# Kernel optimization log

Measured on AMD Instinct MI355X. Metric: run time of the kernel, lower is better.

## Reference

```python
import jax, jax.numpy as jnp
import numpy as np

DIM = 96
NUM_EXPERTS = 4
TOP_K = 1

def setup_inputs() -> dict:
    key = jax.random.key(0)
    ks = jax.random.split(key, 8)
    B, C, H, W = 16, DIM, 128, 128
    E = NUM_EXPERTS
    x = jax.random.normal(ks[0], (B, C, H, W), dtype=jnp.float32)
    # per-expert depthwise 3x3 conv (groups=C): torch weight [C,1,3,3]
    dw_w = jax.random.normal(ks[1], (E, C, 1, 3, 3), dtype=jnp.float32) * 0.1
    dw_b = jax.random.normal(ks[2], (E, C), dtype=jnp.float32) * 0.05
    # per-expert pointwise 1x1 conv: torch weight [C,C,1,1]
    pw_w = jax.random.normal(ks[3], (E, C, C, 1, 1), dtype=jnp.float32) * 0.1
    pw_b = jax.random.normal(ks[4], (E, C), dtype=jnp.float32) * 0.05
    # router linear: torch weight [E, C]
    router_w = jax.random.normal(ks[5], (E, C), dtype=jnp.float32) * 0.1
    router_b = jax.random.normal(ks[6], (E,), dtype=jnp.float32) * 0.05
    return {"x": x, "dw_w": dw_w, "dw_b": dw_b, "pw_w": pw_w, "pw_b": pw_b,
            "router_w": router_w, "router_b": router_b}

def _conv(x, w, groups):
    return jax.lax.conv_general_dilated(
        x, w, window_strides=(1, 1), padding='SAME',
        dimension_numbers=('NCHW', 'OIHW', 'NCHW'),
        feature_group_count=groups)

def _expert(x, dw_w, dw_b, pw_w, pw_b):
    C = x.shape[1]
    h = _conv(x, dw_w, groups=C) + dw_b[None, :, None, None]   # depthwise 3x3
    h = jax.nn.gelu(h, approximate=False)                       # torch GELU (erf)
    return _conv(h, pw_w, groups=1) + pw_b[None, :, None, None] # 1x1 conv

def reference(x, dw_w, dw_b, pw_w, pw_b, router_w, router_b):
    B, C, H, W = x.shape
    E = dw_w.shape[0]
    # router: global avg pool -> linear -> softmax
    pooled = jnp.mean(x, axis=(2, 3))                            # [B, C]
    logits = pooled @ router_w.T + router_b                      # [B, E]
    router_weights = jax.nn.softmax(logits, axis=-1)
    top_weights, top_indices = jax.lax.top_k(router_weights, TOP_K)  # [B, k]
    top_weights = top_weights / (jnp.sum(top_weights, axis=-1, keepdims=True) + 1e-8)
    # run all experts (faithful to the original, which does not dispatch)
    expert_outputs = jnp.stack(
        [_expert(x, dw_w[e], dw_b[e], pw_w[e], pw_b[e]) for e in range(E)],
        axis=1)                                                  # [B, E, C, H, W]
    # scatter top-k weights into dense gates [B, E]
    gates = jnp.zeros((B, E), dtype=x.dtype)
    gates = gates.at[jnp.arange(B)[:, None], top_indices].set(top_weights)
    return jnp.einsum('bechw,be->bchw', expert_outputs, gates)
```

## Files before the change

kernel.cpp:

```cpp
#include <hip/hip_runtime.h>
#include <math.h>

#define DIM 96
#define NE 4
#define HH 128
#define WW 128
#define BB 16
#define KP 24
#define HSROW (KP * 2)
#define HSBUF (WW * HSROW)
#define PWROW 192

typedef __attribute__((ext_vector_type(8))) __bf16 bf16x8;
typedef __attribute__((ext_vector_type(4))) float floatx4;

__device__ __forceinline__ unsigned short f2bf(float f) {
    unsigned u = __builtin_bit_cast(unsigned, f);
    unsigned r = u + 0x7FFFu + ((u >> 16) & 1u);
    return (unsigned short)(r >> 16);
}
__device__ __forceinline__ unsigned pack2(float a, float b) {
    return (unsigned)f2bf(a) | ((unsigned)f2bf(b) << 16);
}

__device__ __forceinline__ float gelu_erf(float h) {
    const float x = h * 0.70710678118654752f;
    const float a = fabsf(x);
    const float t = __builtin_amdgcn_rcpf(__builtin_fmaf(0.3275911f, a, 1.0f));
    float p = __builtin_fmaf(1.061405429f, t, -1.453152027f);
    p = __builtin_fmaf(p, t, 1.421413741f);
    p = __builtin_fmaf(p, t, -0.284496736f);
    p = __builtin_fmaf(p, t, 0.254829592f);
    p *= t;
    const float e = __expf(-x * x);
    float erfv = __builtin_fmaf(-p, e, 1.0f);
    erfv = copysignf(erfv, x);
    return 0.5f * h * (1.0f + erfv);
}

__global__ __launch_bounds__(256) void pool_kernel(const float* __restrict__ x,
                                                   float* __restrict__ pooled) {
    const int bc = blockIdx.x;
    const float4* p = (const float4*)(x + (size_t)bc * (HH * WW));
    const int t = threadIdx.x;
    float s = 0.f;
#pragma unroll
    for (int k = 0; k < (HH * WW / 4) / 256; ++k) {
        float4 v = p[t + k * 256];
        s += v.x + v.y + v.z + v.w;
    }
#pragma unroll
    for (int off = 32; off; off >>= 1) s += __shfl_down(s, off, 64);
    __shared__ float ls[4];
    if ((t & 63) == 0) ls[t >> 6] = s;
    __syncthreads();
    if (t == 0) pooled[bc] = (ls[0] + ls[1] + ls[2] + ls[3]) * (1.0f / (HH * WW));
}

__global__ void router_kernel(const float* __restrict__ pooled,
                              const float* __restrict__ rw,
                              const float* __restrict__ rb,
                              float* __restrict__ gate, int* __restrict__ sel) {
    const int b = threadIdx.x;
    if (b >= BB) return;
    float logits[NE];
#pragma unroll
    for (int e = 0; e < NE; ++e) {
        float s = rb[e];
        for (int c = 0; c < DIM; ++c) s += pooled[b * DIM + c] * rw[e * DIM + c];
        logits[e] = s;
    }
    float m = logits[0];
    int mi = 0;
#pragma unroll
    for (int e = 1; e < NE; ++e)
        if (logits[e] > m) { m = logits[e]; mi = e; }
    float denom = 0.f;
#pragma unroll
    for (int e = 0; e < NE; ++e) denom += expf(logits[e] - m);
    float w = 1.0f / denom;
    gate[b] = w / (w + 1e-8f);
    sel[b] = mi;
}

__device__ __forceinline__ void issue_sub(const float* __restrict__ x, int b,
                                          int cbase, int cg, int rr0, int r,
                                          int rr2, int p4, float4 f[2][3]) {
#pragma unroll
    for (int u = 0; u < 2; ++u) {
        const float* pl = x + (size_t)(b * DIM + cbase + cg * 2 + u) * (HH * WW);
        f[u][0] = *(const float4*)(pl + rr0 * WW + p4);
        f[u][1] = *(const float4*)(pl + r   * WW + p4);
        f[u][2] = *(const float4*)(pl + rr2 * WW + p4);
    }
}

__device__ __forceinline__ void compute_sub(const float4 f[2][3],
                                            const float (*dwc)[12], int cb,
                                            int cg, float lmask, float rmask,
                                            unsigned char* hsbuf, int p4,
                                            unsigned swz) {
    float hq[2][4];
#pragma unroll
    for (int u = 0; u < 2; ++u) {
        const int c = cb + cg * 2 + u;
        const float4 wA = *(const float4*)&dwc[c][0];
        const float4 wB = *(const float4*)&dwc[c][4];
        const float4 wC = *(const float4*)&dwc[c][8];
        float h0 = wC.y, h1 = wC.y, h2 = wC.y, h3 = wC.y;
#pragma unroll
        for (int row = 0; row < 3; ++row) {
            const float ta = (row == 0) ? wA.x : ((row == 1) ? wA.w : wB.z);
            const float tb = (row == 0) ? wA.y : ((row == 1) ? wB.x : wB.w);
            const float tc = (row == 0) ? wA.z : ((row == 1) ? wB.y : wC.x);
            const float4 f4 = f[u][row];
            const float vl = __shfl_up(f4.w, 1, 32) * lmask;
            const float vr = __shfl_down(f4.x, 1, 32) * rmask;
            h0 = __builtin_fmaf(ta, vl,   __builtin_fmaf(tb, f4.x, __builtin_fmaf(tc, f4.y, h0)));
            h1 = __builtin_fmaf(ta, f4.x, __builtin_fmaf(tb, f4.y, __builtin_fmaf(tc, f4.z, h1)));
            h2 = __builtin_fmaf(ta, f4.y, __builtin_fmaf(tb, f4.z, __builtin_fmaf(tc, f4.w, h2)));
            h3 = __builtin_fmaf(ta, f4.z, __builtin_fmaf(tb, f4.w, __builtin_fmaf(tc, vr, h3)));
        }
        hq[u][0] = gelu_erf(h0);
        hq[u][1] = gelu_erf(h1);
        hq[u][2] = gelu_erf(h2);
        hq[u][3] = gelu_erf(h3);
    }
    const unsigned wb0 = (unsigned)(p4 * HSROW + cg * 4);
#pragma unroll
    for (int j = 0; j < 4; ++j) {
        const unsigned off = (wb0 + (unsigned)j * HSROW) ^ swz;
        *(unsigned*)(hsbuf + off) = pack2(hq[0][j], hq[1][j]);
    }
}

__global__ __launch_bounds__(256, 3) void moe_main(
    const float* __restrict__ x, const float* __restrict__ dw_w,
    const float* __restrict__ dw_b, const float* __restrict__ pw_w,
    const float* __restrict__ pw_b, const float* __restrict__ gate,
    const int* __restrict__ sel, float* __restrict__ out) {
    __shared__ __align__(16) unsigned char pwb[DIM * PWROW];
    __shared__ __align__(16) unsigned char hsb[4 * HSBUF];
    __shared__ float dwc[DIM][12];

    const int t = threadIdx.x;
    const unsigned bid = blockIdx.x;
    const int xcd = bid & 7;
    const int s = bid >> 3;
    const int b = s & 15;
    const int r = xcd * 16 + (s >> 4);
    const int e = sel[b];
    const float g = gate[b];

    const int lane = t & 63, w = t >> 6;
    const int wm = w & 1, wn = w >> 1;
    const int ln = lane & 15, kg = lane >> 4;
    const int cobase = wm * 48, pxbase = wn * 64;

    const int g32 = t & 31;
    const int p4 = g32 * 4;
    const int cg = t >> 5;
    const unsigned swz = (unsigned)((g32 & 7) << 4);
    const float lmask = (p4 == 0) ? 0.f : 1.f;
    const float rmask = (p4 == 124) ? 0.f : 1.f;

    const float m0 = (r > 0) ? 1.f : 0.f;
    const float m2 = (r < HH - 1) ? 1.f : 0.f;
    const int rr0 = (r > 0) ? r - 1 : 0;
    const int rr2 = (r < HH - 1) ? r + 1 : HH - 1;

    float4 fA[2][3], fB[2][3];
    issue_sub(x, b, 0, cg, rr0, r, rr2, p4, fA);
    issue_sub(x, b, 16, cg, rr0, r, rr2, p4, fB);

#pragma unroll
    for (int i = 0; i < 18; ++i) {
        const int u = i * 256 + t;
        const int co = u / 48, kp = u - co * 48;
        const float2 v = *(const float2*)(pw_w +
            ((size_t)e * DIM + co) * DIM + kp * 2);
        *(unsigned*)(pwb + ((unsigned)(co * PWROW + kp * 4) ^
                            (unsigned)((co & 7) << 4))) = pack2(v.x, v.y);
    }
    for (int j = t; j < DIM * 12; j += 256) {
        const int c = j / 12, q = j - c * 12;
        float v = 0.f;
        if (q < 9) {
            v = dw_w[((size_t)e * DIM + c) * 9 + q];
            if (q < 3) v *= m0;
            if (q >= 6) v *= m2;
        } else if (q == 9) v = dw_b[e * DIM + c];
        dwc[c][q] = v;
    }
    __syncthreads();

    floatx4 acc[3][4];
#pragma unroll
    for (int i = 0; i < 3; ++i)
#pragma unroll
        for (int j = 0; j < 4; ++j) acc[i][j] = (floatx4){0.f, 0.f, 0.f, 0.f};

#pragma unroll
    for (int pair = 0; pair < 3; ++pair) {
        const int cb = pair * 32;
        unsigned char* h0 = hsb + (unsigned)((pair & 1) * 2) * HSBUF;
        unsigned char* h1 = h0 + HSBUF;
        compute_sub(fA, dwc, cb, cg, lmask, rmask, h0, p4, swz);
        if (pair < 2) issue_sub(x, b, cb + 32, cg, rr0, r, rr2, p4, fA);
        compute_sub(fB, dwc, cb + 16, cg, lmask, rmask, h1, p4, swz);
        if (pair < 2) issue_sub(x, b, cb + 48, cg, rr0, r, rr2, p4, fB);
        __syncthreads();

        const unsigned qbase = (unsigned)((pair & 1) * 2 + (kg >> 1)) * HSBUF;
        bf16x8 af[3], bfr[4];
#pragma unroll
        for (int mf = 0; mf < 3; ++mf) {
            const int co = cobase + mf * 16 + ln;
            af[mf] = *(const bf16x8*)(pwb +
                ((unsigned)(co * PWROW + pair * 64 + kg * 16) ^
                 (unsigned)((co & 7) << 4)));
        }
#pragma unroll
        for (int nf = 0; nf < 4; ++nf) {
            const int pxv = pxbase + nf * 16 + ln;
            const unsigned boff = (unsigned)((pxv * HSROW + (kg & 1) * 16) ^
                                             (((pxv >> 2) & 7) << 4));
            bfr[nf] = *(const bf16x8*)(hsb + qbase + boff);
        }
#pragma unroll
        for (int mf = 0; mf < 3; ++mf)
#pragma unroll
            for (int nf = 0; nf < 4; ++nf)
                acc[mf][nf] = __builtin_amdgcn_mfma_f32_16x16x32_bf16(
                    af[mf], bfr[nf], acc[mf][nf], 0, 0, 0);
    }

#pragma unroll
    for (int mf = 0; mf < 3; ++mf) {
#pragma unroll
        for (int rr = 0; rr < 4; ++rr) {
            const int co = cobase + mf * 16 + kg * 4 + rr;
            const float bias = pw_b[e * DIM + co];
            float* orow = out + ((size_t)(b * DIM + co) * HH + r) * WW;
#pragma unroll
            for (int nf = 0; nf < 4; ++nf)
                orow[pxbase + nf * 16 + ln] = (acc[mf][nf][rr] + bias) * g;
        }
    }
}

extern "C" void kernel_launch(void* const* d_in, const int* in_sizes, int n_in,
                              void* d_out, int out_size, void* d_ws, size_t ws_size,
                              hipStream_t stream) {
    const float* x    = (const float*)d_in[0];
    const float* dw_w = (const float*)d_in[1];
    const float* dw_b = (const float*)d_in[2];
    const float* pw_w = (const float*)d_in[3];
    const float* pw_b = (const float*)d_in[4];
    const float* rw   = (const float*)d_in[5];
    const float* rb   = (const float*)d_in[6];
    float* out = (float*)d_out;

    float* pooled = (float*)d_ws;
    float* gate = pooled + BB * DIM;
    int* sel = (int*)(gate + BB);

    pool_kernel<<<BB * DIM, 256, 0, stream>>>(x, pooled);
    router_kernel<<<1, 64, 0, stream>>>(pooled, rw, rb, gate, sel);
    moe_main<<<HH * BB, 256, 0, stream>>>(x, dw_w, dw_b, pw_w, pw_b, gate, sel, out);
}
```

Baseline: 77.28 us.

## Process two output rows per block to reuse halo rows and pointwise weights

Each block now computes a strip of two image rows instead of one. It loads 4 input rows per channel instead of 3 per row, which cuts redundant halo reads, and it halves how often the pointwise weights are staged into LDS per output. The grid shrinks to half as many blocks and the MFMA accumulator tile doubles to 3x8. Single-buffered LDS needs an extra barrier, and the higher register pressure may lower occupancy under launch_bounds(256,3).

```diff
diff --git a/kernel.cpp b/kernel.cpp
--- a/kernel.cpp
+++ b/kernel.cpp
@@ -6,9 +6,8 @@
 #define HH 128
 #define WW 128
 #define BB 16
-#define KP 24
-#define HSROW (KP * 2)
-#define HSBUF (WW * HSROW)
+#define HSROW 48
+#define HSBUF (256 * HSROW)
 #define PWROW 192
 
 typedef __attribute__((ext_vector_type(8))) __bf16 bf16x8;
@@ -83,54 +82,92 @@
     sel[b] = mi;
 }
 
-__device__ __forceinline__ void issue_sub(const float* __restrict__ x, int b,
-                                          int cbase, int cg, int rr0, int r,
-                                          int rr2, int p4, float4 f[2][3]) {
+__device__ __forceinline__ void issue_sub2(const float* __restrict__ x, int b,
+                                           int cbase, int cg, int rm1, int r0,
+                                           int rp2, int p4, float4 f[2][4]) {
 #pragma unroll
     for (int u = 0; u < 2; ++u) {
         const float* pl = x + (size_t)(b * DIM + cbase + cg * 2 + u) * (HH * WW);
-        f[u][0] = *(const float4*)(pl + rr0 * WW + p4);
-        f[u][1] = *(const float4*)(pl + r   * WW + p4);
-        f[u][2] = *(const float4*)(pl + rr2 * WW + p4);
-    }
-}
-
-__device__ __forceinline__ void compute_sub(const float4 f[2][3],
-                                            const float (*dwc)[12], int cb,
-                                            int cg, float lmask, float rmask,
-                                            unsigned char* hsbuf, int p4,
-                                            unsigned swz) {
-    float hq[2][4];
+        f[u][0] = *(const float4*)(pl + rm1 * WW + p4);
+        f[u][1] = *(const float4*)(pl + r0 * WW + p4);
+        f[u][2] = *(const float4*)(pl + (r0 + 1) * WW + p4);
+        f[u][3] = *(const float4*)(pl + rp2 * WW + p4);
+    }
+}
+
+__device__ __forceinline__ void compute_sub2(const float4 f[2][4],
+                                             const float (*dwc)[12], int cb,
+                                             int cg, float lmask, float rmask,
+                                             float mTop, float mBot,
+                                             unsigned char* hsbuf, int p4,
+                                             unsigned swz) {
+    float hA[2][4], hB[2][4];
 #pragma unroll
     for (int u = 0; u < 2; ++u) {
         const int c = cb + cg * 2 + u;
         const float4 wA = *(const float4*)&dwc[c][0];
         const float4 wB = *(const float4*)&dwc[c][4];
         const float4 wC = *(const float4*)&dwc[c][8];
-        float h0 = wC.y, h1 = wC.y, h2 = wC.y, h3 = wC.y;
-#pragma unroll
-        for (int row = 0; row < 3; ++row) {
-            const float ta = (row == 0) ? wA.x : ((row == 1) ? wA.w : wB.z);
-            const float tb = (row == 0) ? wA.y : ((row == 1) ? wB.x : wB.w);
-            const float tc = (row == 0) ? wA.z : ((row == 1) ? wB.y : wC.x);
-            const float4 f4 = f[u][row];
-            const float vl = __shfl_up(f4.w, 1, 32) * lmask;
-            const float vr = __shfl_down(f4.x, 1, 32) * rmask;
-            h0 = __builtin_fmaf(ta, vl,   __builtin_fmaf(tb, f4.x, __builtin_fmaf(tc, f4.y, h0)));
-            h1 = __builtin_fmaf(ta, f4.x, __builtin_fmaf(tb, f4.y, __builtin_fmaf(tc, f4.z, h1)));
-            h2 = __builtin_fmaf(ta, f4.y, __builtin_fmaf(tb, f4.z, __builtin_fmaf(tc, f4.w, h2)));
-            h3 = __builtin_fmaf(ta, f4.z, __builtin_fmaf(tb, f4.w, __builtin_fmaf(tc, vr, h3)));
-        }
-        hq[u][0] = gelu_erf(h0);
-        hq[u][1] = gelu_erf(h1);
-        hq[u][2] = gelu_erf(h2);
-        hq[u][3] = gelu_erf(h3);
-    }
-    const unsigned wb0 = (unsigned)(p4 * HSROW + cg * 4);
+        const float bs = wC.y;
+        float vl[4], vr[4];
+#pragma unroll
+        for (int k = 0; k < 4; ++k) {
+            vl[k] = __shfl_up(f[u][k].w, 1, 32) * lmask;
+            vr[k] = __shfl_down(f[u][k].x, 1, 32) * rmask;
+        }
+        float a0 = bs, a1 = bs, a2 = bs, a3 = bs;
+        float b0 = bs, b1 = bs, b2 = bs, b3 = bs;
+        {
+            const float ta = wA.x * mTop, tb = wA.y * mTop, tc = wA.z * mTop;
+            const float4 q = f[u][0];
+            a0 = __builtin_fmaf(ta, vl[0], __builtin_fmaf(tb, q.x, __builtin_fmaf(tc, q.y, a0)));
+            a1 = __builtin_fmaf(ta, q.x, __builtin_fmaf(tb, q.y, __builtin_fmaf(tc, q.z, a1)));
+            a2 = __builtin_fmaf(ta, q.y, __builtin_fmaf(tb, q.z, __builtin_fmaf(tc, q.w, a2)));
+            a3 = __builtin_fmaf(ta, q.z, __builtin_fmaf(tb, q.w, __builtin_fmaf(tc, vr[0], a3)));
+        }
+        {
+            const float4 q = f[u][1];
+            a0 = __builtin_fmaf(wA.w, vl[1], __builtin_fmaf(wB.x, q.x, __builtin_fmaf(wB.y, q.y, a0)));
+            a1 = __builtin_fmaf(wA.w, q.x, __builtin_fmaf(wB.x, q.y, __builtin_fmaf(wB.y, q.z, a1)));
+            a2 = __builtin_fmaf(wA.w, q.y, __builtin_fmaf(wB.x, q.z, __builtin_fmaf(wB.y, q.w, a2)));
+            a3 = __builtin_fmaf(wA.w, q.z, __builtin_fmaf(wB.x, q.w, __builtin_fmaf(wB.y, vr[1], a3)));
+            b0 = __builtin_fmaf(wA.x, vl[1], __builtin_fmaf(wA.y, q.x, __builtin_fmaf(wA.z, q.y, b0)));
+            b1 = __builtin_fmaf(wA.x, q.x, __builtin_fmaf(wA.y, q.y, __builtin_fmaf(wA.z, q.z, b1)));
+            b2 = __builtin_fmaf(wA.x, q.y, __builtin_fmaf(wA.y, q.z, __builtin_fmaf(wA.z, q.w, b2)));
+            b3 = __builtin_fmaf(wA.x, q.z, __builtin_fmaf(wA.y, q.w, __builtin_fmaf(wA.z, vr[1], b3)));
+        }
+        {
+            const float4 q = f[u][2];
+            a0 = __builtin_fmaf(wB.z, vl[2], __builtin_fmaf(wB.w, q.x, __builtin_fmaf(wC.x, q.y, a0)));
+            a1 = __builtin_fmaf(wB.z, q.x, __builtin_fmaf(wB.w, q.y, __builtin_fmaf(wC.x, q.z, a1)));
+            a2 = __builtin_fmaf(wB.z, q.y, __builtin_fmaf(wB.w, q.z, __builtin_fmaf(wC.x, q.w, a2)));
+            a3 = __builtin_fmaf(wB.z, q.z, __builtin_fmaf(wB.w, q.w, __builtin_fmaf(wC.x, vr[2], a3)));
+            b0 = __builtin_fmaf(wA.w, vl[2], __builtin_fmaf(wB.x, q.x, __builtin_fmaf(wB.y, q.y, b0)));
+            b1 = __builtin_fmaf(wA.w, q.x, __builtin_fmaf(wB.x, q.y, __builtin_fmaf(wB.y, q.z, b1)));
+            b2 = __builtin_fmaf(wA.w, q.y, __builtin_fmaf(wB.x, q.z, __builtin_fmaf(wB.y, q.w, b2)));
+            b3 = __builtin_fmaf(wA.w, q.z, __builtin_fmaf(wB.x, q.w, __builtin_fmaf(wB.y, vr[2], b3)));
+        }
+        {
+            const float ta = wB.z * mBot, tb = wB.w * mBot, tc = wC.x * mBot;
+            const float4 q = f[u][3];
+            b0 = __builtin_fmaf(ta, vl[3], __builtin_fmaf(tb, q.x, __builtin_fmaf(tc, q.y, b0)));
+            b1 = __builtin_fmaf(ta, q.x, __builtin_fmaf(tb, q.y, __builtin_fmaf(tc, q.z, b1)));
+            b2 = __builtin_fmaf(ta, q.y, __builtin_fmaf(tb, q.z, __builtin_fmaf(tc, q.w, b2)));
+            b3 = __builtin_fmaf(ta, q.z, __builtin_fmaf(tb, q.w, __builtin_fmaf(tc, vr[3], b3)));
+        }
+        hA[u][0] = gelu_erf(a0); hA[u][1] = gelu_erf(a1);
+        hA[u][2] = gelu_erf(a2); hA[u][3] = gelu_erf(a3);
+        hB[u][0] = gelu_erf(b0); hB[u][1] = gelu_erf(b1);
+        hB[u][2] = gelu_erf(b2); hB[u][3] = gelu_erf(b3);
+    }
+    const unsigned wbA = (unsigned)(p4 * HSROW + cg * 4);
+    const unsigned wbB = wbA + 128u * HSROW;
 #pragma unroll
     for (int j = 0; j < 4; ++j) {
-        const unsigned off = (wb0 + (unsigned)j * HSROW) ^ swz;
-        *(unsigned*)(hsbuf + off) = pack2(hq[0][j], hq[1][j]);
+        *(unsigned*)(hsbuf + ((wbA + (unsigned)j * HSROW) ^ swz)) =
+            pack2(hA[0][j], hA[1][j]);
+        *(unsigned*)(hsbuf + ((wbB + (unsigned)j * HSROW) ^ swz)) =
+            pack2(hB[0][j], hB[1][j]);
     }
 }
 
@@ -140,7 +177,7 @@
     const float* __restrict__ pw_b, const float* __restrict__ gate,
     const int* __restrict__ sel, float* __restrict__ out) {
     __shared__ __align__(16) unsigned char pwb[DIM * PWROW];
-    __shared__ __align__(16) unsigned char hsb[4 * HSBUF];
+    __shared__ __align__(16) unsigned char hsb[2 * HSBUF];
     __shared__ float dwc[DIM][12];
 
     const int t = threadIdx.x;
@@ -148,14 +185,15 @@
     const int xcd = bid & 7;
     const int s = bid >> 3;
     const int b = s & 15;
-    const int r = xcd * 16 + (s >> 4);
+    const int strip = xcd * 8 + (s >> 4);
+    const int r0 = strip * 2;
     const int e = sel[b];
     const float g = gate[b];
 
     const int lane = t & 63, w = t >> 6;
     const int wm = w & 1, wn = w >> 1;
     const int ln = lane & 15, kg = lane >> 4;
-    const int cobase = wm * 48, pxbase = wn * 64;
+    const int cobase = wm * 48, pxbase = wn * 128;
 
     const int g32 = t & 31;
     const int p4 = g32 * 4;
@@ -164,14 +202,14 @@
     const float lmask = (p4 == 0) ? 0.f : 1.f;
     const float rmask = (p4 == 124) ? 0.f : 1.f;
 
-    const float m0 = (r > 0) ? 1.f : 0.f;
-    const float m2 = (r < HH - 1) ? 1.f : 0.f;
-    const int rr0 = (r > 0) ? r - 1 : 0;
-    const int rr2 = (r < HH - 1) ? r + 1 : HH - 1;
-
-    float4 fA[2][3], fB[2][3];
-    issue_sub(x, b, 0, cg, rr0, r, rr2, p4, fA);
-    issue_sub(x, b, 16, cg, rr0, r, rr2, p4, fB);
+    const float mTop = (r0 > 0) ? 1.f : 0.f;
+    const float mBot = (r0 < HH - 2) ? 1.f : 0.f;
+    const int rm1 = (r0 > 0) ? r0 - 1 : 0;
+    const int rp2 = (r0 < HH - 2) ? r0 + 2 : HH - 1;
+
+    float4 fA[2][4], fB[2][4];
+    issue_sub2(x, b, 0, cg, rm1, r0, rp2, p4, fA);
+    issue_sub2(x, b, 16, cg, rm1, r0, rp2, p4, fB);
 
 #pragma unroll
     for (int i = 0; i < 18; ++i) {
@@ -185,34 +223,30 @@
     for (int j = t; j < DIM * 12; j += 256) {
         const int c = j / 12, q = j - c * 12;
         float v = 0.f;
-        if (q < 9) {
-            v = dw_w[((size_t)e * DIM + c) * 9 + q];
-            if (q < 3) v *= m0;
-            if (q >= 6) v *= m2;
-        } else if (q == 9) v = dw_b[e * DIM + c];
+        if (q < 9) v = dw_w[((size_t)e * DIM + c) * 9 + q];
+        else if (q == 9) v = dw_b[e * DIM + c];
         dwc[c][q] = v;
     }
     __syncthreads();
 
-    floatx4 acc[3][4];
+    floatx4 acc[3][8];
 #pragma unroll
     for (int i = 0; i < 3; ++i)
 #pragma unroll
-        for (int j = 0; j < 4; ++j) acc[i][j] = (floatx4){0.f, 0.f, 0.f, 0.f};
+        for (int j = 0; j < 8; ++j) acc[i][j] = (floatx4){0.f, 0.f, 0.f, 0.f};
 
 #pragma unroll
     for (int pair = 0; pair < 3; ++pair) {
         const int cb = pair * 32;
-        unsigned char* h0 = hsb + (unsigned)((pair & 1) * 2) * HSBUF;
-        unsigned char* h1 = h0 + HSBUF;
-        compute_sub(fA, dwc, cb, cg, lmask, rmask, h0, p4, swz);
-        if (pair < 2) issue_sub(x, b, cb + 32, cg, rr0, r, rr2, p4, fA);
-        compute_sub(fB, dwc, cb + 16, cg, lmask, rmask, h1, p4, swz);
-        if (pair < 2) issue_sub(x, b, cb + 48, cg, rr0, r, rr2, p4, fB);
+        compute_sub2(fA, dwc, cb, cg, lmask, rmask, mTop, mBot, hsb, p4, swz);
+        if (pair < 2) issue_sub2(x, b, cb + 32, cg, rm1, r0, rp2, p4, fA);
+        compute_sub2(fB, dwc, cb + 16, cg, lmask, rmask, mTop, mBot,
+                     hsb + HSBUF, p4, swz);
+        if (pair < 2) issue_sub2(x, b, cb + 48, cg, rm1, r0, rp2, p4, fB);
         __syncthreads();
 
-        const unsigned qbase = (unsigned)((pair & 1) * 2 + (kg >> 1)) * HSBUF;
-        bf16x8 af[3], bfr[4];
+        const unsigned qbase = (unsigned)(kg >> 1) * HSBUF;
+        bf16x8 af[3], bfr[8];
 #pragma unroll
         for (int mf = 0; mf < 3; ++mf) {
             const int co = cobase + mf * 16 + ln;
@@ -221,7 +255,7 @@
                  (unsigned)((co & 7) << 4)));
         }
 #pragma unroll
-        for (int nf = 0; nf < 4; ++nf) {
+        for (int nf = 0; nf < 8; ++nf) {
             const int pxv = pxbase + nf * 16 + ln;
             const unsigned boff = (unsigned)((pxv * HSROW + (kg & 1) * 16) ^
                                              (((pxv >> 2) & 7) << 4));
@@ -230,9 +264,10 @@
 #pragma unroll
         for (int mf = 0; mf < 3; ++mf)
 #pragma unroll
-            for (int nf = 0; nf < 4; ++nf)
+            for (int nf = 0; nf < 8; ++nf)
                 acc[mf][nf] = __builtin_amdgcn_mfma_f32_16x16x32_bf16(
                     af[mf], bfr[nf], acc[mf][nf], 0, 0, 0);
+        if (pair < 2) __syncthreads();
     }
 
 #pragma unroll
@@ -241,10 +276,12 @@
         for (int rr = 0; rr < 4; ++rr) {
             const int co = cobase + mf * 16 + kg * 4 + rr;
             const float bias = pw_b[e * DIM + co];
-            float* orow = out + ((size_t)(b * DIM + co) * HH + r) * WW;
-#pragma unroll
-            for (int nf = 0; nf < 4; ++nf)
-                orow[pxbase + nf * 16 + ln] = (acc[mf][nf][rr] + bias) * g;
+            float* obase = out + ((size_t)(b * DIM + co) * HH + r0) * WW;
+#pragma unroll
+            for (int nf = 0; nf < 8; ++nf) {
+                const int pxv = pxbase + nf * 16 + ln;
+                obase[(pxv >> 7) * WW + (pxv & 127)] = (acc[mf][nf][rr] + bias) * g;
+            }
         }
     }
 }
@@ -267,5 +304,6 @@
 
     pool_kernel<<<BB * DIM, 256, 0, stream>>>(x, pooled);
     router_kernel<<<1, 64, 0, stream>>>(pooled, rw, rb, gate, sel);
-    moe_main<<<HH * BB, 256, 0, stream>>>(x, dw_w, dw_b, pw_w, pw_b, gate, sel, out);
-}
+    moe_main<<<(HH / 2) * BB, 256, 0, stream>>>(x, dw_w, dw_b, pw_w, pw_b,
+                                                gate, sel, out);
+}
```

New measurement: 112.3 us. +45.4%, slower.
